# Performance work log

Hardware: AMD Instinct MI355X
Metric: run time of the kernel (lower is better)

The kernel has to match this reference:

```python
import jax, jax.numpy as jnp
from jax import lax
import numpy as np

CH = 512      # ch_in = c_in = c_out
P = 8         # p: channels per group
NG = CH // P  # depthwise groups
PG = CH // P  # pointwise groups
EPS = 1e-5
DN = ('NCHW', 'OIHW', 'NCHW')


def leaky(x):
    return jnp.where(x >= 0, x, 0.01 * x)  # LeakyReLU default slope


def setup_inputs() -> dict:
    key = jax.random.key(0)
    ks = jax.random.split(key, 8)
    N, H, W = 16, 64, 64
    return {
        'style_encoding': jax.random.normal(ks[0], (N, 512, 4, 4), jnp.float32),
        'content_in': jax.random.normal(ks[1], (N, CH, H, W), jnp.float32),
        'dw_w': jax.random.normal(ks[2], (P, 512, 2, 2), jnp.float32) * 0.05,
        'dw_b': jax.random.normal(ks[3], (P,), jnp.float32) * 0.05,
        'pk_w': jax.random.normal(ks[4], (P, 512), jnp.float32) * 0.05,
        'pk_b': jax.random.normal(ks[5], (P,), jnp.float32) * 0.05,
        'pb_w': jax.random.normal(ks[6], (CH, 512), jnp.float32) * 0.05,
        'pb_b': jax.random.normal(ks[7], (CH,), jnp.float32) * 0.05,
    }


def reference(style_encoding, content_in, dw_w, dw_b, pk_w, pk_b, pb_w, pb_b):
    N, _, H, W = content_in.shape
    # --- KernelPredictor ---
    # depthwise kernels: 2x2 valid conv on 4x4 style map -> [N, P, 3, 3]
    d = lax.conv_general_dilated(style_encoding, dw_w, (1, 1), 'VALID',
                                 dimension_numbers=DN)
    d = leaky(d + dw_b[None, :, None, None])  # [N, P, 3, 3]
    # expand: same [P,3,3] filter for every output channel -> [N, CH, P, 3, 3]
    depthwise = jnp.broadcast_to(d[:, None], (N, CH, P, 3, 3))
    # avg-pool 4 on 4x4 style map == global mean -> [N, 512]
    s_d = jnp.mean(style_encoding, axis=(2, 3))
    pk = jnp.einsum('nc,oc->no', s_d, pk_w) + pk_b       # [N, P]  (1x1 conv)
    bias = jnp.einsum('nc,oc->no', s_d, pb_w) + pb_b     # [N, CH] (1x1 conv)

    # --- per-sample grouped convs, batched by folding batch into groups ---
    padded = jnp.pad(content_in, ((0, 0), (0, 0), (1, 1), (1, 1)), mode='reflect')
    xr = padded.reshape(1, N * CH, H + 2, W + 2)
    wr = depthwise.reshape(N * CH, P, 3, 3)
    depth = lax.conv_general_dilated(xr, wr, (1, 1), 'VALID',
                                     feature_group_count=N * NG,
                                     dimension_numbers=DN)
    depth = depth.reshape(N, CH, H, W)

    # pointwise 1x1 grouped conv: weight [N, CH, P, 1, 1], identical over out
    # channels within a sample (expand); groups = PG, CH//PG == P out ch/group
    depth_g = depth.reshape(N, PG, P, H, W)
    pw_g = jnp.broadcast_to(pk[:, None, None, :], (N, PG, P, P))  # [n,g,o,j]
    out = jnp.einsum('ngjhw,ngoj->ngohw', depth_g, pw_g).reshape(N, CH, H, W)
    predicted = leaky(out + bias[:, :, None, None])

    # --- instance-norm of content (AdaIN calc_mean_std, unbiased var) ---
    mean = jnp.mean(content_in, axis=(2, 3), keepdims=True)
    std = jnp.sqrt(jnp.var(content_in, axis=(2, 3), keepdims=True, ddof=1) + EPS)
    normalized = (content_in - mean) / std
    return normalized * predicted
```

## Files before the change

### kernel.cpp

```cpp
#include <hip/hip_runtime.h>
#include <math.h>

#define PLANE 4096
#define EPS 1e-5f

#define ROWS 18
#define LDW  68
#define LPLANE (ROWS * LDW)

typedef float f4 __attribute__((ext_vector_type(4)));

__device__ __forceinline__ float leaky(float x) { return x >= 0.f ? x : 0.01f * x; }

__device__ __forceinline__ float wave_sum(float v) {
    #pragma unroll
    for (int off = 32; off; off >>= 1) v += __shfl_xor(v, off, 64);
    return v;
}

__global__ __launch_bounds__(256) void prep_kernel(
    const float* __restrict__ style,
    const float* __restrict__ content,
    const float* __restrict__ dw_w,
    const float* __restrict__ dw_b,
    const float* __restrict__ pk_w,
    const float* __restrict__ pk_b,
    float* __restrict__ sd_out,
    float* __restrict__ S_out,
    float* __restrict__ d_pred,
    float* __restrict__ mean_out,
    float* __restrict__ rstd_out)
{
    const int blk = blockIdx.x;
    const int t = threadIdx.x;
    const int wave = t >> 6, lane = t & 63;

    __shared__ float ls[4], lq[4];
    __shared__ float s_sd[512];
    __shared__ float red[4];

    if (blk < 8192) {
        const float4* base = (const float4*)(content + (size_t)blk * PLANE);
        float s = 0.f, q = 0.f;
        #pragma unroll
        for (int k = 0; k < 4; ++k) {
            float4 v = base[k * 256 + t];
            s += v.x + v.y + v.z + v.w;
            q += v.x * v.x + v.y * v.y + v.z * v.z + v.w * v.w;
        }
        #pragma unroll
        for (int off = 32; off; off >>= 1) {
            s += __shfl_xor(s, off, 64);
            q += __shfl_xor(q, off, 64);
        }
        if (lane == 0) { ls[wave] = s; lq[wave] = q; }
        __syncthreads();
        if (t == 0) {
            float S = ls[0] + ls[1] + ls[2] + ls[3];
            float Q = lq[0] + lq[1] + lq[2] + lq[3];
            float m = S * (1.f / 4096.f);
            float var = (Q - 4096.f * m * m) * (1.f / 4095.f);
            mean_out[blk] = m;
            rstd_out[blk] = rsqrtf(var + EPS);
        }
    } else if (blk < 8208) {
        const int n = blk - 8192;
        const float* sb = style + (size_t)n * 8192;
        #pragma unroll
        for (int qd = 0; qd < 2; ++qd) {
            int c = t + 256 * qd;
            const float4* sp = (const float4*)sb + c * 4;
            float4 a = sp[0], b = sp[1], d = sp[2], e = sp[3];
            float s = a.x + a.y + a.z + a.w + b.x + b.y + b.z + b.w
                    + d.x + d.y + d.z + d.w + e.x + e.y + e.z + e.w;
            s *= (1.f / 16.f);
            s_sd[c] = s;
            sd_out[n * 512 + c] = s;
        }
        __syncthreads();
        float part = 0.f;
        #pragma unroll
        for (int o = 0; o < 8; ++o)
            part += pk_w[o * 512 + t] * s_sd[t]
                  + pk_w[o * 512 + t + 256] * s_sd[t + 256];
        part = wave_sum(part);
        if (lane == 0) red[wave] = part;
        __syncthreads();
        if (t == 0) {
            float S = red[0] + red[1] + red[2] + red[3];
            #pragma unroll
            for (int o = 0; o < 8; ++o) S += pk_b[o];
            S_out[n] = S;
        }
    } else {
        const int n = blk - 8208;
        const float* sb = style + (size_t)n * 8192;
        const float4* wp = (const float4*)dw_w;
        for (int rr = 0; rr < 18; ++rr) {
            int r = wave * 18 + rr;
            int j = r / 9, pos = r % 9, y = pos / 3, x = pos % 3;
            float acc = 0.f;
            #pragma unroll
            for (int i = 0; i < 8; ++i) {
                int c = lane + 64 * i;
                float4 w = wp[j * 512 + c];
                const float* s = sb + c * 16 + y * 4 + x;
                acc += s[0] * w.x + s[1] * w.y + s[4] * w.z + s[5] * w.w;
            }
            acc = wave_sum(acc);
            if (lane == 0) d_pred[n * 72 + r] = leaky(acc + dw_b[j]);
        }
    }
}

__global__ __launch_bounds__(256) void main_kernel(
    const float* __restrict__ content,
    const float* __restrict__ d_pred,
    const float* __restrict__ S_in,
    const float* __restrict__ sd,
    const float* __restrict__ pb_w,
    const float* __restrict__ pb_b,
    const float* __restrict__ mean_in,
    const float* __restrict__ rstd_in,
    float* __restrict__ out)
{
    const int b    = blockIdx.x;
    const int tile = b & 3;
    const int g    = (b >> 2) & 63;
    const int n    = b >> 8;
    const int t  = threadIdx.x;
    const int tx = t & 15, ty = t >> 4;
    const int h  = tile * 16 + ty;
    const int x0 = tx * 4;

    __shared__ float s_x[8 * LPLANE];
    __shared__ float s_d[72];
    __shared__ float s_S;
    __shared__ float s_bias[8], s_mean[8], s_rstd[8];

    if (t < 72) s_d[t] = d_pred[n * 72 + t];
    if (t == 80) s_S = S_in[n];
    if (t >= 96 && t < 104) {
        int o = t - 96;
        int c = n * 512 + g * 8 + o;
        s_mean[o] = mean_in[c];
        s_rstd[o] = rstd_in[c];
    }
    {
        const int o = t >> 5, l = t & 31;
        const float* pw  = pb_w + (size_t)(g * 8 + o) * 512;
        const float* sdn = sd + n * 512;
        float acc = 0.f;
        #pragma unroll
        for (int i = 0; i < 16; ++i) acc += pw[l + 32 * i] * sdn[l + 32 * i];
        #pragma unroll
        for (int off = 16; off; off >>= 1) acc += __shfl_xor(acc, off, 64);
        if (l == 0) s_bias[o] = acc + pb_b[g * 8 + o];
    }

    const float* cbase = content + (size_t)(n * 512 + g * 8) * PLANE;
    #pragma unroll
    for (int i = 0; i < 9; ++i) {
        int q   = t + 256 * i;
        int p   = q / 288;
        int rem = q - p * 288;
        int row = rem >> 4;
        int c4  = rem & 15;
        int y   = tile * 16 + row - 1;
        int ry  = y < 0 ? 1 : (y > 63 ? 62 : y);
        float4 v = *(const float4*)(cbase + p * PLANE + ry * 64 + c4 * 4);
        *(f4*)(s_x + p * LPLANE + row * LDW + c4 * 4) = { v.x, v.y, v.z, v.w };
    }
    __syncthreads();

    const int xmi = (tx == 0)  ? 1  : x0 - 1;
    const int xpi = (tx == 15) ? 62 : x0 + 4;
    float D0 = 0.f, D1 = 0.f, D2 = 0.f, D3 = 0.f;
    #pragma unroll
    for (int j = 0; j < 8; ++j) {
        const float* base = s_x + j * LPLANE;
        #pragma unroll
        for (int r = 0; r < 3; ++r) {
            const float* rowp = base + (ty + r) * LDW;
            f4 v = *(const f4*)(rowp + x0);
            float xm = rowp[xmi];
            float xp = rowp[xpi];
            const float w0 = s_d[j * 9 + r * 3 + 0];
            const float w1 = s_d[j * 9 + r * 3 + 1];
            const float w2 = s_d[j * 9 + r * 3 + 2];
            D0 += w0 * xm  + w1 * v.x + w2 * v.y;
            D1 += w0 * v.x + w1 * v.y + w2 * v.z;
            D2 += w0 * v.y + w1 * v.z + w2 * v.w;
            D3 += w0 * v.z + w1 * v.w + w2 * xp;
        }
    }

    const float S = s_S;
    const float P0 = D0 * S, P1 = D1 * S, P2 = D2 * S, P3 = D3 * S;
    float* obase = out + (size_t)(n * 512 + g * 8) * PLANE + h * 64 + x0;
    #pragma unroll
    for (int o = 0; o < 8; ++o) {
        f4 v = *(const f4*)(s_x + o * LPLANE + (ty + 1) * LDW + x0);
        float bb = s_bias[o], m = s_mean[o], rs = s_rstd[o];
        float4 res;
        res.x = (v.x - m) * rs * leaky(P0 + bb);
        res.y = (v.y - m) * rs * leaky(P1 + bb);
        res.z = (v.z - m) * rs * leaky(P2 + bb);
        res.w = (v.w - m) * rs * leaky(P3 + bb);
        *(float4*)(obase + o * PLANE) = res;
    }
}

extern "C" void kernel_launch(void* const* d_in, const int* in_sizes, int n_in,
                              void* d_out, int out_size, void* d_ws, size_t ws_size,
                              hipStream_t stream) {
    const float* style   = (const float*)d_in[0];
    const float* content = (const float*)d_in[1];
    const float* dw_w    = (const float*)d_in[2];
    const float* dw_b    = (const float*)d_in[3];
    const float* pk_w    = (const float*)d_in[4];
    const float* pk_b    = (const float*)d_in[5];
    const float* pb_w    = (const float*)d_in[6];
    const float* pb_b    = (const float*)d_in[7];
    float* out = (float*)d_out;
    float* ws  = (float*)d_ws;

    const int N = 16;
    float* sd_ws   = ws;
    float* d_pred  = sd_ws + N * 512;
    float* S_ws    = d_pred + N * 72;
    float* mean_ws = S_ws + N;
    float* rstd_ws = mean_ws + N * 512;

    prep_kernel<<<8224, 256, 0, stream>>>(style, content, dw_w, dw_b, pk_w, pk_b,
                                          sd_ws, S_ws, d_pred, mean_ws, rstd_ws);
    main_kernel<<<N * 64 * 4, 256, 0, stream>>>(content, d_pred, S_ws, sd_ws,
                                                pb_w, pb_b, mean_ws, rstd_ws, out);
}
```

Measured before the change: 292.8 us.

## Fuse instance-norm statistics into main kernel, one block per channel group

```diff
diff --git a/kernel.cpp b/kernel.cpp
--- a/kernel.cpp
+++ b/kernel.cpp
@@ -18,53 +18,25 @@
     return v;
 }
 
-__global__ __launch_bounds__(256) void prep_kernel(
+__global__ __launch_bounds__(256) void style_kernel(
     const float* __restrict__ style,
-    const float* __restrict__ content,
     const float* __restrict__ dw_w,
     const float* __restrict__ dw_b,
     const float* __restrict__ pk_w,
     const float* __restrict__ pk_b,
     float* __restrict__ sd_out,
     float* __restrict__ S_out,
-    float* __restrict__ d_pred,
-    float* __restrict__ mean_out,
-    float* __restrict__ rstd_out)
+    float* __restrict__ d_pred)
 {
     const int blk = blockIdx.x;
     const int t = threadIdx.x;
     const int wave = t >> 6, lane = t & 63;
 
-    __shared__ float ls[4], lq[4];
     __shared__ float s_sd[512];
     __shared__ float red[4];
 
-    if (blk < 8192) {
-        const float4* base = (const float4*)(content + (size_t)blk * PLANE);
-        float s = 0.f, q = 0.f;
-        #pragma unroll
-        for (int k = 0; k < 4; ++k) {
-            float4 v = base[k * 256 + t];
-            s += v.x + v.y + v.z + v.w;
-            q += v.x * v.x + v.y * v.y + v.z * v.z + v.w * v.w;
-        }
-        #pragma unroll
-        for (int off = 32; off; off >>= 1) {
-            s += __shfl_xor(s, off, 64);
-            q += __shfl_xor(q, off, 64);
-        }
-        if (lane == 0) { ls[wave] = s; lq[wave] = q; }
-        __syncthreads();
-        if (t == 0) {
-            float S = ls[0] + ls[1] + ls[2] + ls[3];
-            float Q = lq[0] + lq[1] + lq[2] + lq[3];
-            float m = S * (1.f / 4096.f);
-            float var = (Q - 4096.f * m * m) * (1.f / 4095.f);
-            mean_out[blk] = m;
-            rstd_out[blk] = rsqrtf(var + EPS);
-        }
-    } else if (blk < 8208) {
-        const int n = blk - 8192;
+    if (blk < 16) {
+        const int n = blk;
         const float* sb = style + (size_t)n * 8192;
         #pragma unroll
         for (int qd = 0; qd < 2; ++qd) {
@@ -93,7 +65,7 @@
             S_out[n] = S;
         }
     } else {
-        const int n = blk - 8208;
+        const int n = blk - 16;
         const float* sb = style + (size_t)n * 8192;
         const float4* wp = (const float4*)dw_w;
         for (int rr = 0; rr < 18; ++rr) {
@@ -113,25 +85,21 @@
     }
 }
 
-__global__ __launch_bounds__(256) void main_kernel(
+__global__ __launch_bounds__(256, 4) void main_kernel(
     const float* __restrict__ content,
     const float* __restrict__ d_pred,
     const float* __restrict__ S_in,
     const float* __restrict__ sd,
     const float* __restrict__ pb_w,
     const float* __restrict__ pb_b,
-    const float* __restrict__ mean_in,
-    const float* __restrict__ rstd_in,
     float* __restrict__ out)
 {
-    const int b    = blockIdx.x;
-    const int tile = b & 3;
-    const int g    = (b >> 2) & 63;
-    const int n    = b >> 8;
-    const int t  = threadIdx.x;
+    const int b = blockIdx.x;
+    const int g = b & 63, n = b >> 6;
+    const int t = threadIdx.x;
     const int tx = t & 15, ty = t >> 4;
-    const int h  = tile * 16 + ty;
     const int x0 = tx * 4;
+    const int wave = t >> 6, lane = t & 63;
 
     __shared__ float s_x[8 * LPLANE];
     __shared__ float s_d[72];
@@ -140,12 +108,6 @@
 
     if (t < 72) s_d[t] = d_pred[n * 72 + t];
     if (t == 80) s_S = S_in[n];
-    if (t >= 96 && t < 104) {
-        int o = t - 96;
-        int c = n * 512 + g * 8 + o;
-        s_mean[o] = mean_in[c];
-        s_rstd[o] = rstd_in[c];
-    }
     {
         const int o = t >> 5, l = t & 31;
         const float* pw  = pb_w + (size_t)(g * 8 + o) * 512;
@@ -160,54 +122,81 @@
 
     const float* cbase = content + (size_t)(n * 512 + g * 8) * PLANE;
     #pragma unroll
-    for (int i = 0; i < 9; ++i) {
-        int q   = t + 256 * i;
-        int p   = q / 288;
-        int rem = q - p * 288;
-        int row = rem >> 4;
-        int c4  = rem & 15;
-        int y   = tile * 16 + row - 1;
-        int ry  = y < 0 ? 1 : (y > 63 ? 62 : y);
-        float4 v = *(const float4*)(cbase + p * PLANE + ry * 64 + c4 * 4);
-        *(f4*)(s_x + p * LPLANE + row * LDW + c4 * 4) = { v.x, v.y, v.z, v.w };
+    for (int jj = 0; jj < 2; ++jj) {
+        const int j = wave * 2 + jj;
+        const float4* p = (const float4*)(cbase + j * PLANE);
+        float s = 0.f, q = 0.f;
+        #pragma unroll 4
+        for (int k = 0; k < 16; ++k) {
+            float4 v = p[lane + 64 * k];
+            s += v.x + v.y + v.z + v.w;
+            q += v.x * v.x + v.y * v.y + v.z * v.z + v.w * v.w;
+        }
+        s = wave_sum(s);
+        q = wave_sum(q);
+        if (lane == 0) {
+            float m = s * (1.f / 4096.f);
+            float var = (q - 4096.f * m * m) * (1.f / 4095.f);
+            s_mean[j] = m;
+            s_rstd[j] = rsqrtf(var + EPS);
+        }
     }
     __syncthreads();
 
-    const int xmi = (tx == 0)  ? 1  : x0 - 1;
-    const int xpi = (tx == 15) ? 62 : x0 + 4;
-    float D0 = 0.f, D1 = 0.f, D2 = 0.f, D3 = 0.f;
-    #pragma unroll
-    for (int j = 0; j < 8; ++j) {
-        const float* base = s_x + j * LPLANE;
-        #pragma unroll
-        for (int r = 0; r < 3; ++r) {
-            const float* rowp = base + (ty + r) * LDW;
-            f4 v = *(const f4*)(rowp + x0);
-            float xm = rowp[xmi];
-            float xp = rowp[xpi];
-            const float w0 = s_d[j * 9 + r * 3 + 0];
-            const float w1 = s_d[j * 9 + r * 3 + 1];
-            const float w2 = s_d[j * 9 + r * 3 + 2];
-            D0 += w0 * xm  + w1 * v.x + w2 * v.y;
-            D1 += w0 * v.x + w1 * v.y + w2 * v.z;
-            D2 += w0 * v.y + w1 * v.z + w2 * v.w;
-            D3 += w0 * v.z + w1 * v.w + w2 * xp;
-        }
-    }
-
     const float S = s_S;
-    const float P0 = D0 * S, P1 = D1 * S, P2 = D2 * S, P3 = D3 * S;
-    float* obase = out + (size_t)(n * 512 + g * 8) * PLANE + h * 64 + x0;
-    #pragma unroll
-    for (int o = 0; o < 8; ++o) {
-        f4 v = *(const f4*)(s_x + o * LPLANE + (ty + 1) * LDW + x0);
-        float bb = s_bias[o], m = s_mean[o], rs = s_rstd[o];
-        float4 res;
-        res.x = (v.x - m) * rs * leaky(P0 + bb);
-        res.y = (v.y - m) * rs * leaky(P1 + bb);
-        res.z = (v.z - m) * rs * leaky(P2 + bb);
-        res.w = (v.w - m) * rs * leaky(P3 + bb);
-        *(float4*)(obase + o * PLANE) = res;
+    #pragma unroll 1
+    for (int tile = 0; tile < 4; ++tile) {
+        #pragma unroll
+        for (int i = 0; i < 9; ++i) {
+            int q   = t + 256 * i;
+            int p   = q / 288;
+            int rem = q - p * 288;
+            int row = rem >> 4;
+            int c4  = rem & 15;
+            int y   = tile * 16 + row - 1;
+            int ry  = y < 0 ? 1 : (y > 63 ? 62 : y);
+            float4 v = *(const float4*)(cbase + p * PLANE + ry * 64 + c4 * 4);
+            *(f4*)(s_x + p * LPLANE + row * LDW + c4 * 4) = { v.x, v.y, v.z, v.w };
+        }
+        __syncthreads();
+
+        const int xmi = (tx == 0)  ? 1  : x0 - 1;
+        const int xpi = (tx == 15) ? 62 : x0 + 4;
+        float D0 = 0.f, D1 = 0.f, D2 = 0.f, D3 = 0.f;
+        #pragma unroll
+        for (int j = 0; j < 8; ++j) {
+            const float* base = s_x + j * LPLANE;
+            #pragma unroll
+            for (int r = 0; r < 3; ++r) {
+                const float* rowp = base + (ty + r) * LDW;
+                f4 v = *(const f4*)(rowp + x0);
+                float xm = rowp[xmi];
+                float xp = rowp[xpi];
+                const float w0 = s_d[j * 9 + r * 3 + 0];
+                const float w1 = s_d[j * 9 + r * 3 + 1];
+                const float w2 = s_d[j * 9 + r * 3 + 2];
+                D0 += w0 * xm  + w1 * v.x + w2 * v.y;
+                D1 += w0 * v.x + w1 * v.y + w2 * v.z;
+                D2 += w0 * v.y + w1 * v.z + w2 * v.w;
+                D3 += w0 * v.z + w1 * v.w + w2 * xp;
+            }
+        }
+
+        const float P0 = D0 * S, P1 = D1 * S, P2 = D2 * S, P3 = D3 * S;
+        const int h = tile * 16 + ty;
+        float* obase = out + (size_t)(n * 512 + g * 8) * PLANE + h * 64 + x0;
+        #pragma unroll
+        for (int o = 0; o < 8; ++o) {
+            f4 v = *(const f4*)(s_x + o * LPLANE + (ty + 1) * LDW + x0);
+            float bb = s_bias[o], m = s_mean[o], rs = s_rstd[o];
+            f4 res;
+            res.x = (v.x - m) * rs * leaky(P0 + bb);
+            res.y = (v.y - m) * rs * leaky(P1 + bb);
+            res.z = (v.z - m) * rs * leaky(P2 + bb);
+            res.w = (v.w - m) * rs * leaky(P3 + bb);
+            __builtin_nontemporal_store(res, (f4*)(obase + o * PLANE));
+        }
+        __syncthreads();
     }
 }
 
@@ -226,14 +215,12 @@
     float* ws  = (float*)d_ws;
 
     const int N = 16;
-    float* sd_ws   = ws;
-    float* d_pred  = sd_ws + N * 512;
-    float* S_ws    = d_pred + N * 72;
-    float* mean_ws = S_ws + N;
-    float* rstd_ws = mean_ws + N * 512;
-
-    prep_kernel<<<8224, 256, 0, stream>>>(style, content, dw_w, dw_b, pk_w, pk_b,
-                                          sd_ws, S_ws, d_pred, mean_ws, rstd_ws);
-    main_kernel<<<N * 64 * 4, 256, 0, stream>>>(content, d_pred, S_ws, sd_ws,
-                                                pb_w, pb_b, mean_ws, rstd_ws, out);
-}
+    float* sd_ws  = ws;
+    float* d_pred = sd_ws + N * 512;
+    float* S_ws   = d_pred + N * 72;
+
+    style_kernel<<<32, 256, 0, stream>>>(style, dw_w, dw_b, pk_w, pk_b,
+                                         sd_ws, S_ws, d_pred);
+    main_kernel<<<N * 64, 256, 0, stream>>>(content, d_pred, S_ws, sd_ws,
+                                            pb_w, pb_b, out);
+}
```

Measured after the change: 325.8 us. 11.3% more time.
